# Performance work log

Hardware: AMD Instinct MI355X
Metric: run time of the kernel (lower is better)

The kernel has to match this reference:

```python
import jax, jax.numpy as jnp
import numpy as np

B, S, D = 8, 2048, 1024
TEMPERATURE = 32.0  # sqrt(d_model)
NEG_INF = -1e16


def setup_inputs() -> dict:
    key = jax.random.key(0)
    ks = jax.random.split(key, 9)
    sc = 1.0 / np.sqrt(D)
    q = jax.random.normal(ks[0], (B, S, D), dtype=jnp.float32)
    k = jax.random.normal(ks[1], (B, S, D), dtype=jnp.float32)
    v = jax.random.normal(ks[2], (B, S, D), dtype=jnp.float32)
    # nn.Linear weights are [out, in]; init roughly uniform(-1/sqrt(in), 1/sqrt(in))
    Wq = jax.random.uniform(ks[3], (D, D), jnp.float32, -sc, sc)
    Wk = jax.random.uniform(ks[4], (D, D), jnp.float32, -sc, sc)
    Wv = jax.random.uniform(ks[5], (D, D), jnp.float32, -sc, sc)
    bq = jax.random.uniform(ks[6], (D,), jnp.float32, -sc, sc)
    bk = jax.random.uniform(ks[7], (D,), jnp.float32, -sc, sc)
    bv = jax.random.uniform(ks[8], (D,), jnp.float32, -sc, sc)
    # causal mask: True where attention is DISALLOWED (masked_fill semantics)
    mask = jnp.triu(jnp.ones((S, S), dtype=bool), k=1)
    mask = jnp.broadcast_to(mask[None, :, :], (B, S, S))
    return {"q": q, "k": k, "v": v, "Wq": Wq, "bq": bq, "Wk": Wk,
            "bk": bk, "Wv": Wv, "bv": bv, "mask": mask}


def reference(q, k, v, Wq, bq, Wk, bk, Wv, bv, mask):
    # Linear projections (torch Linear: x @ W.T + b)
    qp = jnp.einsum('bsd,ed->bse', q, Wq) + bq  # [B,S,D]
    kp = jnp.einsum('bsd,ed->bse', k, Wk) + bk
    vp = jnp.einsum('bsd,ed->bse', v, Wv) + bv
    # scores [B,S,S]
    attn = jnp.einsum('bsd,btd->bst', qp, kp) / TEMPERATURE
    attn = jnp.where(mask, NEG_INF, attn)
    attn = jax.nn.softmax(attn, axis=2)
    # dropout p=0.0 -> identity (eval mode)
    output = jnp.einsum('bst,btd->bsd', attn, vp)  # [B,S,D]
    return (output, attn)
```

## Files before the change

### kernel.cpp

```cpp
#include <hip/hip_runtime.h>
#include <hip/hip_bf16.h>
#include <stdint.h>

#define SEQ 2048
#define DIM 1024
#define NB  8

typedef __attribute__((ext_vector_type(8))) __bf16 bf16x8;
typedef __attribute__((ext_vector_type(8))) unsigned short ushort8;
typedef __attribute__((ext_vector_type(4))) float f32x4;

__device__ inline unsigned short f2b(float f) {
  union { float f; uint32_t u; } c; c.f = f;
  uint32_t u = c.u;
  return (unsigned short)((u + 0x7fffu + ((u >> 16) & 1u)) >> 16);
}

__device__ inline void async16(const void* g, void* l) {
  __builtin_amdgcn_global_load_lds((const __attribute__((address_space(1))) uint32_t*)g,
                                   (__attribute__((address_space(3))) uint32_t*)l,
                                   16, 0, 0);
}

__global__ __launch_bounds__(256) void cvt_f32_bf16(const float* __restrict__ in,
                                                    unsigned short* __restrict__ out, int n4) {
  int idx = blockIdx.x * 256 + threadIdx.x;
  int stride = gridDim.x * 256;
  for (int i = idx; i < n4; i += stride) {
    float4 f = ((const float4*)in)[i];
    ushort4 h;
    h.x = f2b(f.x); h.y = f2b(f.y); h.z = f2b(f.z); h.w = f2b(f.w);
    ((ushort4*)out)[i] = h;
  }
}

template<int MODE>
__global__ __launch_bounds__(256)
void gemm_nt(const unsigned short* __restrict__ A,
             const unsigned short* __restrict__ B,
             void* __restrict__ Cv,
             const float* __restrict__ bias,
             int K, int lda, int ldb, int ldc,
             long long aStride, long long bStride, long long cStride,
             float scale)
{
  if (MODE == 1 && blockIdx.y > blockIdx.x) return;
  __shared__ __align__(16) unsigned short lA[128 * 32];
  __shared__ __align__(16) unsigned short lB[128 * 32];
  const int bm0 = blockIdx.x * 128;
  const int bn0 = blockIdx.y * 128;
  const int z = blockIdx.z;
  A += (long long)z * aStride;
  B += (long long)z * bStride;
  const int tid  = threadIdx.x;
  const int lane = tid & 63;
  const int wv   = tid >> 6;
  const int wm   = (wv >> 1) * 64;
  const int wn   = (wv & 1) * 64;
  const int l15  = lane & 15;
  const int l4   = lane >> 4;
  const int Keff = (MODE == 2) ? (bm0 + 128) : K;

  f32x4 acc[4][4] = {};

  const int srow = tid >> 2;
  const int skb  = (tid & 3) * 16;
  const char* gA = (const char*)A + ((size_t)(bm0 + srow) * lda) * 2 + skb;
  const char* gB = (const char*)B + ((size_t)(bn0 + srow) * ldb) * 2 + skb;
  const size_t stepA = (size_t)64 * lda * 2;
  const size_t stepB = (size_t)64 * ldb * 2;

  for (int k0 = 0; k0 < Keff; k0 += 32) {
    const char* ga = gA + (size_t)k0 * 2;
    const char* gb = gB + (size_t)k0 * 2;
    async16(ga,         &lA[tid * 8]);
    async16(ga + stepA, &lA[(tid + 256) * 8]);
    async16(gb,         &lB[tid * 8]);
    async16(gb + stepB, &lB[(tid + 256) * 8]);
    __syncthreads();
    bf16x8 af[4], bfr[4];
    #pragma unroll
    for (int i = 0; i < 4; ++i)
      af[i] = __builtin_bit_cast(bf16x8, *(const ushort8*)&lA[(wm + i*16 + l15) * 32 + l4 * 8]);
    #pragma unroll
    for (int j = 0; j < 4; ++j)
      bfr[j] = __builtin_bit_cast(bf16x8, *(const ushort8*)&lB[(wn + j*16 + l15) * 32 + l4 * 8]);
    #pragma unroll
    for (int i = 0; i < 4; ++i)
      #pragma unroll
      for (int j = 0; j < 4; ++j)
        acc[i][j] = __builtin_amdgcn_mfma_f32_16x16x32_bf16(af[i], bfr[j], acc[i][j], 0, 0, 0);
    __syncthreads();
  }

  if (MODE == 0) {
    unsigned short* Ch = (unsigned short*)Cv;
    #pragma unroll
    for (int i = 0; i < 4; ++i)
      #pragma unroll
      for (int r = 0; r < 4; ++r) {
        int row = bm0 + wm + i * 16 + l4 * 4 + r;
        #pragma unroll
        for (int j = 0; j < 4; ++j) {
          int col = bn0 + wn + j * 16 + l15;
          Ch[(size_t)row * ldc + col] = f2b(acc[i][j][r] + bias[col]);
        }
      }
  } else {
    float* Cf = (float*)Cv + (long long)z * cStride;
    #pragma unroll
    for (int i = 0; i < 4; ++i)
      #pragma unroll
      for (int r = 0; r < 4; ++r) {
        int row = bm0 + wm + i * 16 + l4 * 4 + r;
        #pragma unroll
        for (int j = 0; j < 4; ++j) {
          int col = bn0 + wn + j * 16 + l15;
          Cf[(size_t)row * ldc + col] = acc[i][j][r] * scale;
        }
      }
  }
}

__global__ __launch_bounds__(256)
void softmax_causal(float* __restrict__ attnF, unsigned short* __restrict__ attnH) {
  const int S = SEQ;
  int row = blockIdx.x;
  int i = row & (S - 1);
  float* rp = attnF + (size_t)row * S;
  unsigned short* hp = attnH + (size_t)row * S;
  int len = i + 1;
  int tid = threadIdx.x;
  float vals[8];
  float m = -1e30f;
  #pragma unroll
  for (int it = 0; it < 8; ++it) {
    int j = it * 256 + tid;
    float v = (j < len) ? rp[j] : -1e30f;
    vals[it] = v;
    m = fmaxf(m, v);
  }
  #pragma unroll
  for (int o = 32; o > 0; o >>= 1) m = fmaxf(m, __shfl_xor(m, o, 64));
  __shared__ float red[4];
  int wv = tid >> 6, lane = tid & 63;
  if (lane == 0) red[wv] = m;
  __syncthreads();
  m = fmaxf(fmaxf(red[0], red[1]), fmaxf(red[2], red[3]));
  __syncthreads();
  float s = 0.f;
  #pragma unroll
  for (int it = 0; it < 8; ++it) {
    float e = __expf(vals[it] - m);
    vals[it] = e;
    s += e;
  }
  #pragma unroll
  for (int o = 32; o > 0; o >>= 1) s += __shfl_xor(s, o, 64);
  if (lane == 0) red[wv] = s;
  __syncthreads();
  s = red[0] + red[1] + red[2] + red[3];
  float inv = 1.f / s;
  #pragma unroll
  for (int it = 0; it < 8; ++it) {
    float o = vals[it] * inv;
    rp[it * 256 + tid] = o;
    hp[it * 256 + tid] = f2b(o);
  }
}

__global__ void transpose_bf16(const unsigned short* __restrict__ in, unsigned short* __restrict__ out) {
  __shared__ unsigned short tile[32][33];
  size_t zoff = (size_t)blockIdx.z * SEQ * DIM;
  const unsigned short* ip = in + zoff;
  unsigned short* op = out + zoff;
  int c0 = blockIdx.x * 32;
  int r0 = blockIdx.y * 32;
  int tx = threadIdx.x, ty = threadIdx.y;
  #pragma unroll
  for (int dy = 0; dy < 32; dy += 8)
    tile[ty + dy][tx] = ip[(size_t)(r0 + ty + dy) * DIM + c0 + tx];
  __syncthreads();
  #pragma unroll
  for (int dy = 0; dy < 32; dy += 8)
    op[(size_t)(c0 + ty + dy) * SEQ + r0 + tx] = tile[tx][ty + dy];
}

extern "C" void kernel_launch(void* const* d_in, const int* in_sizes, int n_in,
                              void* d_out, int out_size, void* d_ws, size_t ws_size,
                              hipStream_t stream) {
  (void)in_sizes; (void)n_in; (void)out_size; (void)ws_size;
  const int B = NB, S = SEQ, D = DIM;
  const size_t BSD = (size_t)B * S * D;
  const size_t BSS = (size_t)B * S * S;
  const size_t DD  = (size_t)D * D;

  const float* q  = (const float*)d_in[0];
  const float* k  = (const float*)d_in[1];
  const float* v  = (const float*)d_in[2];
  const float* Wq = (const float*)d_in[3];
  const float* bq = (const float*)d_in[4];
  const float* Wk = (const float*)d_in[5];
  const float* bk = (const float*)d_in[6];
  const float* Wv = (const float*)d_in[7];
  const float* bv = (const float*)d_in[8];

  float* out   = (float*)d_out;
  float* attnF = out + BSD;

  unsigned short* xb  = (unsigned short*)d_ws;
  unsigned short* Wqb = xb + BSD;
  unsigned short* Wkb = Wqb + DD;
  unsigned short* Wvb = Wkb + DD;
  unsigned short* qp  = Wvb + DD;
  unsigned short* kp  = qp + BSD;
  unsigned short* vp  = kp + BSD;
  unsigned short* attnH = vp;

  dim3 blk(256);
  cvt_f32_bf16<<<dim3(512), blk, 0, stream>>>(Wq, Wqb, (int)(DD / 4));
  cvt_f32_bf16<<<dim3(512), blk, 0, stream>>>(Wk, Wkb, (int)(DD / 4));
  cvt_f32_bf16<<<dim3(512), blk, 0, stream>>>(Wv, Wvb, (int)(DD / 4));
  cvt_f32_bf16<<<dim3(4096), blk, 0, stream>>>(q, xb, (int)(BSD / 4));
  gemm_nt<0><<<dim3(128, 8, 1), blk, 0, stream>>>(xb, Wqb, qp, bq, D, D, D, D, 0, 0, 0, 1.f);
  cvt_f32_bf16<<<dim3(4096), blk, 0, stream>>>(k, xb, (int)(BSD / 4));
  gemm_nt<0><<<dim3(128, 8, 1), blk, 0, stream>>>(xb, Wkb, kp, bk, D, D, D, D, 0, 0, 0, 1.f);
  cvt_f32_bf16<<<dim3(4096), blk, 0, stream>>>(v, xb, (int)(BSD / 4));
  gemm_nt<0><<<dim3(128, 8, 1), blk, 0, stream>>>(xb, Wvb, vp, bv, D, D, D, D, 0, 0, 0, 1.f);
  transpose_bf16<<<dim3(D / 32, S / 32, B), dim3(32, 8), 0, stream>>>(vp, xb);
  gemm_nt<1><<<dim3(S / 128, S / 128, B), blk, 0, stream>>>(qp, kp, attnF, nullptr,
      D, D, D, S, (long long)S * D, (long long)S * D, (long long)S * S, 1.f / 32.f);
  softmax_causal<<<dim3(B * S), blk, 0, stream>>>(attnF, attnH);
  gemm_nt<2><<<dim3(S / 128, D / 128, B), blk, 0, stream>>>(attnH, xb, out, nullptr,
      S, S, S, D, (long long)S * S, (long long)D * S, (long long)S * D, 1.f);
}
```

Baseline: 849.5 us.

## Double-buffer LDS tiles in GEMM and add grouped block-index swizzle

Each k-step's async global-to-LDS loads now go into one of two shared-memory buffers, so the next tile's load is issued before computing on the current one. This removes the trailing barrier and overlaps memory latency with MFMA work, at the cost of double the LDS per block. Block indices are also remapped in groups of 8 M-tiles so that concurrently running blocks share A/B tiles in L2. The causal-skip and causal K-limit checks now use the remapped tile coordinates.

```diff
diff --git a/kernel.cpp b/kernel.cpp
--- a/kernel.cpp
+++ b/kernel.cpp
@@ -32,6 +32,17 @@
     h.x = f2b(f.x); h.y = f2b(f.y); h.z = f2b(f.z); h.w = f2b(f.w);
     ((ushort4*)out)[i] = h;
   }
+}
+
+__device__ inline void remap_mn(int& bm, int& bn) {
+  const int mT = gridDim.x, nT = gridDim.y;
+  int did = blockIdx.y * mT + blockIdx.x;
+  const int GM = 8;
+  int per = GM * nT;
+  int group = did / per;
+  int rem = did - group * per;
+  bm = group * GM + (rem % GM);
+  bn = rem / GM;
 }
 
 template<int MODE>
@@ -44,11 +55,13 @@
              long long aStride, long long bStride, long long cStride,
              float scale)
 {
-  if (MODE == 1 && blockIdx.y > blockIdx.x) return;
-  __shared__ __align__(16) unsigned short lA[128 * 32];
-  __shared__ __align__(16) unsigned short lB[128 * 32];
-  const int bm0 = blockIdx.x * 128;
-  const int bn0 = blockIdx.y * 128;
+  __shared__ __align__(16) unsigned short lA[2][128 * 32];
+  __shared__ __align__(16) unsigned short lB[2][128 * 32];
+  int bm, bn;
+  remap_mn(bm, bn);
+  if (MODE == 1 && bn > bm) return;
+  const int bm0 = bm * 128;
+  const int bn0 = bn * 128;
   const int z = blockIdx.z;
   A += (long long)z * aStride;
   B += (long long)z * bStride;
@@ -70,27 +83,33 @@
   const size_t stepA = (size_t)64 * lda * 2;
   const size_t stepB = (size_t)64 * ldb * 2;
 
-  for (int k0 = 0; k0 < Keff; k0 += 32) {
+  auto stage = [&](int buf, int k0) {
     const char* ga = gA + (size_t)k0 * 2;
     const char* gb = gB + (size_t)k0 * 2;
-    async16(ga,         &lA[tid * 8]);
-    async16(ga + stepA, &lA[(tid + 256) * 8]);
-    async16(gb,         &lB[tid * 8]);
-    async16(gb + stepB, &lB[(tid + 256) * 8]);
+    async16(ga,         &lA[buf][tid * 8]);
+    async16(ga + stepA, &lA[buf][(tid + 256) * 8]);
+    async16(gb,         &lB[buf][tid * 8]);
+    async16(gb + stepB, &lB[buf][(tid + 256) * 8]);
+  };
+
+  stage(0, 0);
+  int buf = 0;
+  for (int k0 = 0; k0 < Keff; k0 += 32) {
     __syncthreads();
+    if (k0 + 32 < Keff) stage(buf ^ 1, k0 + 32);
     bf16x8 af[4], bfr[4];
     #pragma unroll
     for (int i = 0; i < 4; ++i)
-      af[i] = __builtin_bit_cast(bf16x8, *(const ushort8*)&lA[(wm + i*16 + l15) * 32 + l4 * 8]);
+      af[i] = __builtin_bit_cast(bf16x8, *(const ushort8*)&lA[buf][(wm + i*16 + l15) * 32 + l4 * 8]);
     #pragma unroll
     for (int j = 0; j < 4; ++j)
-      bfr[j] = __builtin_bit_cast(bf16x8, *(const ushort8*)&lB[(wn + j*16 + l15) * 32 + l4 * 8]);
+      bfr[j] = __builtin_bit_cast(bf16x8, *(const ushort8*)&lB[buf][(wn + j*16 + l15) * 32 + l4 * 8]);
     #pragma unroll
     for (int i = 0; i < 4; ++i)
       #pragma unroll
       for (int j = 0; j < 4; ++j)
         acc[i][j] = __builtin_amdgcn_mfma_f32_16x16x32_bf16(af[i], bfr[j], acc[i][j], 0, 0, 0);
-    __syncthreads();
+    buf ^= 1;
   }
 
   if (MODE == 0) {
```

Measured after the change: 768.1 us. -9.6%, faster.
